# Kernel tuning notes

Measured on AMD Instinct MI355X. Metric: run time of the kernel, lower is better.

Reference implementation:

```python
import jax, jax.numpy as jnp
import numpy as np

EPS = 1e-10      # normalizer eps from the torch module
IN_EPS = 1e-5    # torch InstanceNorm2d default eps
STRIDE = 2
PAD = 1


def _dw_conv_transpose(x, W):
    """Depthwise ConvTranspose2d applied for every output channel at once.

    x: [B, Cin, H, W]
    W: [Cin, Cout, kh, kw]  (W[:, i] is sub_convs[i].weight of shape [Cin, 1, kh, kw])
    returns: [B, Cin, Cout, H', W'] where channel (c, i) = convT of x[:, c] with W[c, i].
    """
    Cin, Cout, kh, kw = W.shape
    # Transposed conv == dilated conv with spatially flipped kernel,
    # lhs_dilation = stride, padding = k - 1 - pad (output_padding = 0).
    rhs = jnp.flip(W, axis=(-2, -1)).reshape(Cin * Cout, 1, kh, kw)
    pad_h = (kh - 1 - PAD, kh - 1 - PAD)
    pad_w = (kw - 1 - PAD, kw - 1 - PAD)
    out = jax.lax.conv_general_dilated(
        x, rhs,
        window_strides=(1, 1),
        padding=(pad_h, pad_w),
        lhs_dilation=(STRIDE, STRIDE),
        dimension_numbers=('NCHW', 'OIHW', 'NCHW'),
        feature_group_count=Cin,
    )  # [B, Cin*Cout, H', W'], group-major: group c -> channels c*Cout:(c+1)*Cout
    B = x.shape[0]
    return out.reshape(B, Cin, Cout, out.shape[2], out.shape[3])


def setup_inputs() -> dict:
    key = jax.random.key(0)
    k1, k2, k3 = jax.random.split(key, 3)
    B, Cin, Cout, H, Wd, K = 2, 64, 64, 48, 48, 4
    x = jax.random.normal(k1, (B, Cin, H, Wd), dtype=jnp.float32)
    # Positive-leaning weights keep the normalizer (convT of ones) away from zero.
    W = 0.05 + 0.1 * jax.random.uniform(k2, (Cin, Cout, K, K), dtype=jnp.float32)
    bias = 0.02 * jax.random.normal(k3, (Cout,), dtype=jnp.float32)
    return {"x": x, "W": W, "bias": bias}


def reference(x, W, bias):
    # numerator: depthwise convT of the input for every (in_ch, out_ch) pair
    num = _dw_conv_transpose(x, W)                       # [B, Cin, Cout, H', W']
    # normalizer: same convT applied to ones (batch-independent -> batch of 1)
    den = _dw_conv_transpose(jnp.ones_like(x[:1]), W) + EPS  # [1, Cin, Cout, H', W']
    out = jnp.sum(num / den, axis=1) + bias[None, :, None, None]  # [B, Cout, H', W']
    # InstanceNorm2d (no affine, biased variance) over spatial dims per (b, c)
    mean = jnp.mean(out, axis=(2, 3), keepdims=True)
    var = jnp.var(out, axis=(2, 3), keepdims=True)
    return (out - mean) / jnp.sqrt(var + IN_EPS)
```

## Files before the change

### kernel.cpp

```cpp
#include <hip/hip_runtime.h>

#define BB    2
#define CIN   64
#define NI    64
#define HIN   48
#define WIN   48
#define HO    96
#define WO    96
#define EPSN  1e-10f
#define IN_EPS 1e-5f
#define IMG   (HO*WO)
#define NIMG  (BB*NI)

#define XTROW 50
#define XTSL  (XTROW*XTROW*64)

using half8  = __attribute__((ext_vector_type(8))) _Float16;
using half2v = __attribute__((ext_vector_type(2))) _Float16;
using f32x4  = __attribute__((ext_vector_type(4))) float;

__device__ _Float16 g_xt[BB * XTSL];
__device__ _Float16 g_G[16 * 64 * 64];
__device__ float    g_out[NIMG * IMG];

__global__ __launch_bounds__(256) void prep_kernel(const float* __restrict__ x,
                                                   const float* __restrict__ Wt) {
    const int blk = blockIdx.x;
    const int tid = threadIdx.x;

    if (blk < 96) {
        const int b = blk / 48, h = blk - 48 * b, hp = h + 1;
        __shared__ float sT[64][49];
        for (int e = tid; e < 64 * 12; e += 256) {
            const int c = e / 12, w4 = e - 12 * c;
            const float4 t = *(const float4*)(x + ((size_t)(b * 64 + c) * 48 + h) * 48 + 4 * w4);
            sT[c][4 * w4]     = t.x;
            sT[c][4 * w4 + 1] = t.y;
            sT[c][4 * w4 + 2] = t.z;
            sT[c][4 * w4 + 3] = t.w;
        }
        __syncthreads();
        _Float16* xr = g_xt + (size_t)b * XTSL + (size_t)hp * (XTROW * 64);
        for (int e = tid; e < XTROW * 32; e += 256) {
            const int wp = e >> 5, cp = e & 31;
            half2v hv;
            if (wp == 0 || wp == 49) { hv[0] = (_Float16)0.f; hv[1] = (_Float16)0.f; }
            else { hv[0] = (_Float16)sT[2 * cp][wp - 1]; hv[1] = (_Float16)sT[2 * cp + 1][wp - 1]; }
            *(half2v*)(xr + wp * 64 + 2 * cp) = hv;
        }
        return;
    }
    if (blk < 100) {
        const int z = blk - 96;
        const int b = z >> 1, hp = (z & 1) ? 49 : 0;
        _Float16* xr = g_xt + (size_t)b * XTSL + (size_t)hp * (XTROW * 64);
        half2v hz; hz[0] = (_Float16)0.f; hz[1] = (_Float16)0.f;
        for (int e = tid; e < XTROW * 32; e += 256)
            *(half2v*)(xr + (e >> 5) * 64 + 2 * (e & 31)) = hz;
        return;
    }
    const int combo = blk - 100;
    const int py = combo >> 3, px = (combo >> 2) & 1, a = (combo >> 1) & 1, bb = combo & 1;
    const int kh = 2 * a + 1 - py, kw = 2 * bb + 1 - px;
    for (int e = tid; e < 4096; e += 256) {
        const int i = e >> 6, c = e & 63;
        const float* wp = Wt + ((size_t)c * NI + i) * 16;
        float den = 0.f;
#pragma unroll
        for (int a2 = 0; a2 < 2; ++a2)
#pragma unroll
            for (int b2 = 0; b2 < 2; ++b2)
                den += wp[(2 * a2 + 1 - py) * 4 + (2 * b2 + 1 - px)];
        g_G[combo * 4096 + e] = (_Float16)(wp[kh * 4 + kw] / (den + EPSN));
    }
}

__global__ __launch_bounds__(64) void gemm_kernel() {
    const int blk = blockIdx.x;
    const int t0 = blk & 1;
    int rest = blk >> 1;
    const int n0 = (rest % 3) * 16; rest /= 3;
    const int r = rest % 48;
    const int b = rest / 48;
    const int i0 = 32 * t0;
    const int lane = threadIdx.x;
    const int il = lane & 15, q = lane >> 4;

    f32x4 acc[4][2];
#pragma unroll
    for (int p = 0; p < 4; ++p)
#pragma unroll
        for (int n = 0; n < 2; ++n) { acc[p][n][0] = 0.f; acc[p][n][1] = 0.f; acc[p][n][2] = 0.f; acc[p][n][3] = 0.f; }

    const _Float16* xbase = g_xt + (size_t)b * XTSL
                          + ((size_t)(r + 1) * XTROW + (n0 + il + 1)) * 64 + q * 8;
    const _Float16* gbase = g_G + (i0 + il) * 64 + q * 8;

#pragma unroll
    for (int khalf = 0; khalf < 2; ++khalf) {
        const int ko = khalf * 32;
        half8 A[3][3];
#pragma unroll
        for (int dr = 0; dr < 3; ++dr)
#pragma unroll
            for (int dc = 0; dc < 3; ++dc)
                A[dr][dc] = *(const half8*)(xbase + (dr - 1) * (XTROW * 64) + (dc - 1) * 64 + ko);

#pragma unroll
        for (int combo = 0; combo < 16; ++combo) {
            const int py = combo >> 3, px = (combo >> 2) & 1;
            const int a = (combo >> 1) & 1, bb = combo & 1;
            const int pi = combo >> 2;
            const half8 B0 = *(const half8*)(gbase + combo * 4096 + ko);
            const half8 B1 = *(const half8*)(gbase + combo * 4096 + 1024 + ko);
            const half8 Af = A[py - a + 1][px - bb + 1];
            acc[pi][0] = __builtin_amdgcn_mfma_f32_16x16x32_f16(Af, B0, acc[pi][0], 0, 0, 0);
            acc[pi][1] = __builtin_amdgcn_mfma_f32_16x16x32_f16(Af, B1, acc[pi][1], 0, 0, 0);
        }
    }

#pragma unroll
    for (int pi = 0; pi < 4; ++pi) {
        const int py = pi >> 1, px = pi & 1;
        const int y = 2 * r + py;
#pragma unroll
        for (int nt = 0; nt < 2; ++nt) {
            float* ob = g_out + (size_t)(b * 64 + i0 + 16 * nt + il) * IMG
                      + y * WO + 2 * n0 + 8 * q + px;
#pragma unroll
            for (int reg = 0; reg < 4; ++reg)
                ob[2 * reg] = acc[pi][nt][reg];
        }
    }
}

__global__ __launch_bounds__(256) void epilogue_kernel(
        const float* __restrict__ Wt, const float* __restrict__ bias,
        float* __restrict__ out) {
    const int bi = blockIdx.x;
    const int b = bi >> 6, i = bi & 63;
    const int tid = threadIdx.x;

    __shared__ float sWb[16 * 4 * 64];
    __shared__ float sFix[384];
    __shared__ float sRed[10];

    for (int e = tid; e < 4096; e += 256) {
        const int cls = e >> 8, t = (e >> 6) & 3, c = e & 63;
        const int cy = cls >> 2, cx = cls & 3;
        const float* wp = Wt + ((size_t)c * NI + i) * 16;
        const int THn[4] = {1, 2, 2, 1};
        const int THv[4][2] = {{1, 1}, {0, 2}, {1, 3}, {2, 2}};
        float den = 0.f;
        for (int aa = 0; aa < THn[cy]; ++aa)
            for (int bb = 0; bb < THn[cx]; ++bb)
                den += wp[THv[cy][aa] * 4 + THv[cx][bb]];
        const int khA = (cy & 1) ? 0 : 1, kwA = (cx & 1) ? 0 : 1;
        const int kh = (t >> 1) ? khA + 2 : khA;
        const int kw = (t & 1) ? kwA + 2 : kwA;
        sWb[e] = wp[kh * 4 + kw] / (den + EPSN);
    }
    __syncthreads();

    const _Float16* xb = g_xt + (size_t)b * XTSL;
#pragma unroll
    for (int k = 0; k < 2; ++k) {
        const int p = tid + 256 * k;
        if (p >= 380) break;
        int y, xo;
        if (p < 96)       { y = 0;            xo = p; }
        else if (p < 192) { y = 95;           xo = p - 96; }
        else if (p < 286) { y = p - 192 + 1;  xo = 0; }
        else              { y = p - 286 + 1;  xo = 95; }
        const int hpA = ((y + 1) >> 1) + 1, hpB = hpA - 1;
        const int wpA = ((xo + 1) >> 1) + 1, wpB = wpA - 1;
        const int cy = (y == 0) ? 0 : (y == 95) ? 3 : ((y & 1) ? 1 : 2);
        const int cx = (xo == 0) ? 0 : (xo == 95) ? 3 : ((xo & 1) ? 1 : 2);
        const float* w0 = &sWb[(cy * 4 + cx) * 256];
        const _Float16* pAA = xb + (hpA * XTROW + wpA) * 64;
        const _Float16* pAB = xb + (hpA * XTROW + wpB) * 64;
        const _Float16* pBA = xb + (hpB * XTROW + wpA) * 64;
        const _Float16* pBB = xb + (hpB * XTROW + wpB) * 64;
        float acc = 0.f;
#pragma unroll 8
        for (int c = 0; c < 64; ++c)
            acc += (float)pAA[c] * w0[c]       + (float)pAB[c] * w0[64 + c]
                 + (float)pBA[c] * w0[128 + c] + (float)pBB[c] * w0[192 + c];
        sFix[p] = acc;
    }
    __syncthreads();

    const float bv = bias[i];
    const float4* gb = (const float4*)(g_out + (size_t)bi * IMG);
    float4 v[9];
    float s1 = 0.f, s2 = 0.f;
#pragma unroll
    for (int k = 0; k < 9; ++k) {
        const int idx = k * 256 + tid;
        float4 t = gb[idx];
        const int p = 4 * idx;
        const int y = p / 96, xq = p - 96 * y;
        if (y == 0)       { t.x = sFix[xq]; t.y = sFix[xq + 1]; t.z = sFix[xq + 2]; t.w = sFix[xq + 3]; }
        else if (y == 95) { t.x = sFix[96 + xq]; t.y = sFix[97 + xq]; t.z = sFix[98 + xq]; t.w = sFix[99 + xq]; }
        else {
            if (xq == 0)  t.x = sFix[192 + y - 1];
            if (xq == 92) t.w = sFix[286 + y - 1];
        }
        t.x += bv; t.y += bv; t.z += bv; t.w += bv;
        v[k] = t;
        s1 += t.x + t.y + t.z + t.w;
        s2 += t.x * t.x + t.y * t.y + t.z * t.z + t.w * t.w;
    }

#pragma unroll
    for (int off = 32; off > 0; off >>= 1) {
        s1 += __shfl_down(s1, off, 64);
        s2 += __shfl_down(s2, off, 64);
    }
    const int w = tid >> 6;
    if ((tid & 63) == 0) { sRed[w] = s1; sRed[4 + w] = s2; }
    __syncthreads();
    if (tid == 0) {
        const float t1 = sRed[0] + sRed[1] + sRed[2] + sRed[3];
        const float t2 = sRed[4] + sRed[5] + sRed[6] + sRed[7];
        const float mean = t1 * (1.f / 9216.f);
        const float m2 = t2 * (1.f / 9216.f);
        sRed[8] = mean;
        sRed[9] = rsqrtf(m2 - mean * mean + IN_EPS);
    }
    __syncthreads();
    const float mean = sRed[8], inv = sRed[9];

    float4* ob = (float4*)out + (size_t)bi * (IMG / 4);
#pragma unroll
    for (int k = 0; k < 9; ++k) {
        float4 t = v[k];
        t.x = (t.x - mean) * inv; t.y = (t.y - mean) * inv;
        t.z = (t.z - mean) * inv; t.w = (t.w - mean) * inv;
        ob[k * 256 + tid] = t;
    }
}

extern "C" void kernel_launch(void* const* d_in, const int* in_sizes, int n_in,
                              void* d_out, int out_size, void* d_ws, size_t ws_size,
                              hipStream_t stream) {
    const float* x    = (const float*)d_in[0];
    const float* Wt   = (const float*)d_in[1];
    const float* bias = (const float*)d_in[2];
    float* out = (float*)d_out;
    (void)d_ws; (void)ws_size;

    prep_kernel<<<116, 256, 0, stream>>>(x, Wt);
    gemm_kernel<<<576, 64, 0, stream>>>();
    epilogue_kernel<<<128, 256, 0, stream>>>(Wt, bias, out);
}
```

Before: 101.0 us.

## Split GEMM over K halves, move border fixup into prep, widen epilogue

The GEMM kernel now splits the 64-channel reduction into two halves across separate blocks, doubling the grid to 1152 wavefronts. Each half writes its own partial output buffer, and the epilogue sums the two partials. The border fixup, now computed from the fp32 input with a per-channel normalizer, moves into 128 extra blocks of the prep kernel, so the epilogue only loads precomputed fix values and runs with 768 threads per block. This adds parallelism and shortens the epilogue's critical path, at the cost of an extra 9.4MB of partial-output writes and reads.

```diff
diff --git a/kernel.cpp b/kernel.cpp
--- a/kernel.cpp
+++ b/kernel.cpp
@@ -21,7 +21,8 @@
 
 __device__ _Float16 g_xt[BB * XTSL];
 __device__ _Float16 g_G[16 * 64 * 64];
-__device__ float    g_out[NIMG * IMG];
+__device__ float    g_out2[2][NIMG * IMG];
+__device__ float    g_fix[NIMG * 384];
 
 __global__ __launch_bounds__(256) void prep_kernel(const float* __restrict__ x,
                                                    const float* __restrict__ Wt) {
@@ -59,110 +60,35 @@
             *(half2v*)(xr + (e >> 5) * 64 + 2 * (e & 31)) = hz;
         return;
     }
-    const int combo = blk - 100;
-    const int py = combo >> 3, px = (combo >> 2) & 1, a = (combo >> 1) & 1, bb = combo & 1;
-    const int kh = 2 * a + 1 - py, kw = 2 * bb + 1 - px;
-    for (int e = tid; e < 4096; e += 256) {
-        const int i = e >> 6, c = e & 63;
-        const float* wp = Wt + ((size_t)c * NI + i) * 16;
-        float den = 0.f;
-#pragma unroll
-        for (int a2 = 0; a2 < 2; ++a2)
-#pragma unroll
-            for (int b2 = 0; b2 < 2; ++b2)
-                den += wp[(2 * a2 + 1 - py) * 4 + (2 * b2 + 1 - px)];
-        g_G[combo * 4096 + e] = (_Float16)(wp[kh * 4 + kw] / (den + EPSN));
-    }
-}
-
-__global__ __launch_bounds__(64) void gemm_kernel() {
-    const int blk = blockIdx.x;
-    const int t0 = blk & 1;
-    int rest = blk >> 1;
-    const int n0 = (rest % 3) * 16; rest /= 3;
-    const int r = rest % 48;
-    const int b = rest / 48;
-    const int i0 = 32 * t0;
-    const int lane = threadIdx.x;
-    const int il = lane & 15, q = lane >> 4;
-
-    f32x4 acc[4][2];
-#pragma unroll
-    for (int p = 0; p < 4; ++p)
-#pragma unroll
-        for (int n = 0; n < 2; ++n) { acc[p][n][0] = 0.f; acc[p][n][1] = 0.f; acc[p][n][2] = 0.f; acc[p][n][3] = 0.f; }
-
-    const _Float16* xbase = g_xt + (size_t)b * XTSL
-                          + ((size_t)(r + 1) * XTROW + (n0 + il + 1)) * 64 + q * 8;
-    const _Float16* gbase = g_G + (i0 + il) * 64 + q * 8;
-
-#pragma unroll
-    for (int khalf = 0; khalf < 2; ++khalf) {
-        const int ko = khalf * 32;
-        half8 A[3][3];
-#pragma unroll
-        for (int dr = 0; dr < 3; ++dr)
-#pragma unroll
-            for (int dc = 0; dc < 3; ++dc)
-                A[dr][dc] = *(const half8*)(xbase + (dr - 1) * (XTROW * 64) + (dc - 1) * 64 + ko);
-
-#pragma unroll
-        for (int combo = 0; combo < 16; ++combo) {
-            const int py = combo >> 3, px = (combo >> 2) & 1;
-            const int a = (combo >> 1) & 1, bb = combo & 1;
-            const int pi = combo >> 2;
-            const half8 B0 = *(const half8*)(gbase + combo * 4096 + ko);
-            const half8 B1 = *(const half8*)(gbase + combo * 4096 + 1024 + ko);
-            const half8 Af = A[py - a + 1][px - bb + 1];
-            acc[pi][0] = __builtin_amdgcn_mfma_f32_16x16x32_f16(Af, B0, acc[pi][0], 0, 0, 0);
-            acc[pi][1] = __builtin_amdgcn_mfma_f32_16x16x32_f16(Af, B1, acc[pi][1], 0, 0, 0);
-        }
-    }
-
-#pragma unroll
-    for (int pi = 0; pi < 4; ++pi) {
-        const int py = pi >> 1, px = pi & 1;
-        const int y = 2 * r + py;
-#pragma unroll
-        for (int nt = 0; nt < 2; ++nt) {
-            float* ob = g_out + (size_t)(b * 64 + i0 + 16 * nt + il) * IMG
-                      + y * WO + 2 * n0 + 8 * q + px;
-#pragma unroll
-            for (int reg = 0; reg < 4; ++reg)
-                ob[2 * reg] = acc[pi][nt][reg];
-        }
-    }
-}
-
-__global__ __launch_bounds__(256) void epilogue_kernel(
-        const float* __restrict__ Wt, const float* __restrict__ bias,
-        float* __restrict__ out) {
-    const int bi = blockIdx.x;
+    if (blk < 116) {
+        const int combo = blk - 100;
+        const int py = combo >> 3, px = (combo >> 2) & 1, a = (combo >> 1) & 1, bb = combo & 1;
+        const int kh = 2 * a + 1 - py, kw = 2 * bb + 1 - px;
+        for (int e = tid; e < 4096; e += 256) {
+            const int i = e >> 6, c = e & 63;
+            const float* wp = Wt + ((size_t)c * NI + i) * 16;
+            float den = 0.f;
+#pragma unroll
+            for (int a2 = 0; a2 < 2; ++a2)
+#pragma unroll
+                for (int b2 = 0; b2 < 2; ++b2)
+                    den += wp[(2 * a2 + 1 - py) * 4 + (2 * b2 + 1 - px)];
+            g_G[combo * 4096 + e] = (_Float16)(wp[kh * 4 + kw] / (den + EPSN));
+        }
+        return;
+    }
+
+    const int bi = blk - 116;
     const int b = bi >> 6, i = bi & 63;
-    const int tid = threadIdx.x;
-
-    __shared__ float sWb[16 * 4 * 64];
-    __shared__ float sFix[384];
-    __shared__ float sRed[10];
-
-    for (int e = tid; e < 4096; e += 256) {
-        const int cls = e >> 8, t = (e >> 6) & 3, c = e & 63;
-        const int cy = cls >> 2, cx = cls & 3;
-        const float* wp = Wt + ((size_t)c * NI + i) * 16;
-        const int THn[4] = {1, 2, 2, 1};
-        const int THv[4][2] = {{1, 1}, {0, 2}, {1, 3}, {2, 2}};
-        float den = 0.f;
-        for (int aa = 0; aa < THn[cy]; ++aa)
-            for (int bb = 0; bb < THn[cx]; ++bb)
-                den += wp[THv[cy][aa] * 4 + THv[cx][bb]];
-        const int khA = (cy & 1) ? 0 : 1, kwA = (cx & 1) ? 0 : 1;
-        const int kh = (t >> 1) ? khA + 2 : khA;
-        const int kw = (t & 1) ? kwA + 2 : kwA;
-        sWb[e] = wp[kh * 4 + kw] / (den + EPSN);
-    }
-    __syncthreads();
-
-    const _Float16* xb = g_xt + (size_t)b * XTSL;
+    __shared__ float sWt[64 * 16];
+    {
+        const int c = tid >> 2, q = tid & 3;
+        *(float4*)&sWt[c * 16 + 4 * q] =
+            *(const float4*)(Wt + ((size_t)c * NI + i) * 16 + 4 * q);
+    }
+    __syncthreads();
+
+    const float* xb = x + (size_t)b * (64 * HIN * WIN);
 #pragma unroll
     for (int k = 0; k < 2; ++k) {
         const int p = tid + 256 * k;
@@ -172,32 +98,117 @@
         else if (p < 192) { y = 95;           xo = p - 96; }
         else if (p < 286) { y = p - 192 + 1;  xo = 0; }
         else              { y = p - 286 + 1;  xo = 95; }
-        const int hpA = ((y + 1) >> 1) + 1, hpB = hpA - 1;
-        const int wpA = ((xo + 1) >> 1) + 1, wpB = wpA - 1;
+        const int hA = (y + 1) >> 1, hB = hA - 1;
+        const int khA = (y & 1) ? 0 : 1, khB = khA + 2;
+        const int wA = (xo + 1) >> 1, wB = wA - 1;
+        const int kwA = (xo & 1) ? 0 : 1, kwB = kwA + 2;
+        const bool okA = hA < HIN, okB = hB >= 0;
+        const bool okC = wA < WIN, okD = wB >= 0;
+        const int hAc = okA ? hA : 0, hBc = okB ? hB : 0;
+        const int wAc = okC ? wA : 0, wBc = okD ? wB : 0;
         const int cy = (y == 0) ? 0 : (y == 95) ? 3 : ((y & 1) ? 1 : 2);
         const int cx = (xo == 0) ? 0 : (xo == 95) ? 3 : ((xo & 1) ? 1 : 2);
-        const float* w0 = &sWb[(cy * 4 + cx) * 256];
-        const _Float16* pAA = xb + (hpA * XTROW + wpA) * 64;
-        const _Float16* pAB = xb + (hpA * XTROW + wpB) * 64;
-        const _Float16* pBA = xb + (hpB * XTROW + wpA) * 64;
-        const _Float16* pBB = xb + (hpB * XTROW + wpB) * 64;
+        const int THn[4] = {1, 2, 2, 1};
+        const int THv[4][2] = {{1, 1}, {0, 2}, {1, 3}, {2, 2}};
         float acc = 0.f;
-#pragma unroll 8
-        for (int c = 0; c < 64; ++c)
-            acc += (float)pAA[c] * w0[c]       + (float)pAB[c] * w0[64 + c]
-                 + (float)pBA[c] * w0[128 + c] + (float)pBB[c] * w0[192 + c];
-        sFix[p] = acc;
-    }
-    __syncthreads();
-
-    const float bv = bias[i];
-    const float4* gb = (const float4*)(g_out + (size_t)bi * IMG);
-    float4 v[9];
+        for (int c = 0; c < 64; ++c) {
+            const float* wc = &sWt[c * 16];
+            float den = 0.f;
+            for (int aa = 0; aa < THn[cy]; ++aa)
+                for (int bb = 0; bb < THn[cx]; ++bb)
+                    den += wc[THv[cy][aa] * 4 + THv[cx][bb]];
+            const float* xc = xb + (size_t)c * (HIN * WIN);
+            float num = 0.f;
+            if (okA & okC) num += xc[hAc * WIN + wAc] * wc[khA * 4 + kwA];
+            if (okA & okD) num += xc[hAc * WIN + wBc] * wc[khA * 4 + kwB];
+            if (okB & okC) num += xc[hBc * WIN + wAc] * wc[khB * 4 + kwA];
+            if (okB & okD) num += xc[hBc * WIN + wBc] * wc[khB * 4 + kwB];
+            acc += num / (den + EPSN);
+        }
+        g_fix[bi * 384 + p] = acc;
+    }
+}
+
+__global__ __launch_bounds__(64) void gemm_kernel() {
+    const int blk = blockIdx.x;
+    const int khalf = blk & 1;
+    int rest = blk >> 1;
+    const int t0 = rest & 1; rest >>= 1;
+    const int n0 = (rest % 3) * 16; rest /= 3;
+    const int r = rest % 48;
+    const int b = rest / 48;
+    const int i0 = 32 * t0;
+    const int lane = threadIdx.x;
+    const int il = lane & 15, q = lane >> 4;
+    const int ko = khalf * 32;
+
+    f32x4 acc[4][2];
+#pragma unroll
+    for (int p = 0; p < 4; ++p)
+#pragma unroll
+        for (int n = 0; n < 2; ++n) { acc[p][n][0] = 0.f; acc[p][n][1] = 0.f; acc[p][n][2] = 0.f; acc[p][n][3] = 0.f; }
+
+    const _Float16* xbase = g_xt + (size_t)b * XTSL
+                          + ((size_t)(r + 1) * XTROW + (n0 + il + 1)) * 64 + q * 8 + ko;
+    const _Float16* gbase = g_G + (i0 + il) * 64 + q * 8 + ko;
+
+    half8 A[3][3];
+#pragma unroll
+    for (int dr = 0; dr < 3; ++dr)
+#pragma unroll
+        for (int dc = 0; dc < 3; ++dc)
+            A[dr][dc] = *(const half8*)(xbase + (dr - 1) * (XTROW * 64) + (dc - 1) * 64);
+
+#pragma unroll
+    for (int combo = 0; combo < 16; ++combo) {
+        const int py = combo >> 3, px = (combo >> 2) & 1;
+        const int a = (combo >> 1) & 1, bb = combo & 1;
+        const int pi = combo >> 2;
+        const half8 B0 = *(const half8*)(gbase + combo * 4096);
+        const half8 B1 = *(const half8*)(gbase + combo * 4096 + 1024);
+        const half8 Af = A[py - a + 1][px - bb + 1];
+        acc[pi][0] = __builtin_amdgcn_mfma_f32_16x16x32_f16(Af, B0, acc[pi][0], 0, 0, 0);
+        acc[pi][1] = __builtin_amdgcn_mfma_f32_16x16x32_f16(Af, B1, acc[pi][1], 0, 0, 0);
+    }
+
+#pragma unroll
+    for (int pi = 0; pi < 4; ++pi) {
+        const int py = pi >> 1, px = pi & 1;
+        const int y = 2 * r + py;
+#pragma unroll
+        for (int nt = 0; nt < 2; ++nt) {
+            float* ob = g_out2[khalf] + (size_t)(b * 64 + i0 + 16 * nt + il) * IMG
+                      + y * WO + 2 * n0 + 8 * q + px;
+#pragma unroll
+            for (int reg = 0; reg < 4; ++reg)
+                ob[2 * reg] = acc[pi][nt][reg];
+        }
+    }
+}
+
+__global__ __launch_bounds__(768) void epilogue_kernel(
+        const float* __restrict__ bias, float* __restrict__ out) {
+    const int bi = blockIdx.x;
+    const int tid = threadIdx.x;
+    const float bv = bias[bi & 63];
+
+    __shared__ float sFix[384];
+    __shared__ float red[24];
+    __shared__ float stat[2];
+    if (tid < 384) sFix[tid] = g_fix[bi * 384 + tid];
+    __syncthreads();
+
+    const float4* p0 = (const float4*)(g_out2[0] + (size_t)bi * IMG);
+    const float4* p1 = (const float4*)(g_out2[1] + (size_t)bi * IMG);
+
+    float4 v[3];
     float s1 = 0.f, s2 = 0.f;
 #pragma unroll
-    for (int k = 0; k < 9; ++k) {
-        const int idx = k * 256 + tid;
-        float4 t = gb[idx];
+    for (int k = 0; k < 3; ++k) {
+        const int idx = k * 768 + tid;
+        const float4 a = p0[idx], c = p1[idx];
+        float4 t;
+        t.x = a.x + c.x; t.y = a.y + c.y; t.z = a.z + c.z; t.w = a.w + c.w;
         const int p = 4 * idx;
         const int y = p / 96, xq = p - 96 * y;
         if (y == 0)       { t.x = sFix[xq]; t.y = sFix[xq + 1]; t.z = sFix[xq + 2]; t.w = sFix[xq + 3]; }
@@ -218,26 +229,28 @@
         s2 += __shfl_down(s2, off, 64);
     }
     const int w = tid >> 6;
-    if ((tid & 63) == 0) { sRed[w] = s1; sRed[4 + w] = s2; }
+    if ((tid & 63) == 0) { red[w] = s1; red[12 + w] = s2; }
     __syncthreads();
     if (tid == 0) {
-        const float t1 = sRed[0] + sRed[1] + sRed[2] + sRed[3];
-        const float t2 = sRed[4] + sRed[5] + sRed[6] + sRed[7];
+        float t1 = 0.f, t2 = 0.f;
+#pragma unroll
+        for (int k = 0; k < 12; ++k) { t1 += red[k]; t2 += red[12 + k]; }
         const float mean = t1 * (1.f / 9216.f);
         const float m2 = t2 * (1.f / 9216.f);
-        sRed[8] = mean;
-        sRed[9] = rsqrtf(m2 - mean * mean + IN_EPS);
-    }
-    __syncthreads();
-    const float mean = sRed[8], inv = sRed[9];
+        stat[0] = mean;
+        stat[1] = rsqrtf(m2 - mean * mean + IN_EPS);
+    }
+    __syncthreads();
+    const float mean = stat[0], inv = stat[1];
 
     float4* ob = (float4*)out + (size_t)bi * (IMG / 4);
 #pragma unroll
-    for (int k = 0; k < 9; ++k) {
+    for (int k = 0; k < 3; ++k) {
+        const int idx = k * 768 + tid;
         float4 t = v[k];
         t.x = (t.x - mean) * inv; t.y = (t.y - mean) * inv;
         t.z = (t.z - mean) * inv; t.w = (t.w - mean) * inv;
-        ob[k * 256 + tid] = t;
+        ob[idx] = t;
     }
 }
 
@@ -250,7 +263,7 @@
     float* out = (float*)d_out;
     (void)d_ws; (void)ws_size;
 
-    prep_kernel<<<116, 256, 0, stream>>>(x, Wt);
-    gemm_kernel<<<576, 64, 0, stream>>>();
-    epilogue_kernel<<<128, 256, 0, stream>>>(Wt, bias, out);
-}
+    prep_kernel<<<244, 256, 0, stream>>>(x, Wt);
+    gemm_kernel<<<1152, 64, 0, stream>>>();
+    epilogue_kernel<<<128, 768, 0, stream>>>(bias, out);
+}
```

Result: slower. 205.3 us (+103.2%).
